# Optimization experiments

Measured on AMD Instinct MI355X. Metric: run time of the kernel, lower is better.

The kernel has to match this reference:

```python
import jax, jax.numpy as jnp
import numpy as np

ALPHA = 0.2  # LeakyReLU negative slope

def setup_inputs() -> dict:
    key = jax.random.key(0)
    k1, k2, k3 = jax.random.split(key, 3)
    B, N, D_in, D_out = 4, 512, 512, 256
    H = jax.random.normal(k1, (B, N, D_in), dtype=jnp.float32)
    # xavier-style scaled params
    W = jax.random.normal(k2, (D_out, D_in), dtype=jnp.float32) * (2.0 / (D_in + D_out)) ** 0.5
    a = jax.random.normal(k3, (D_out, 1), dtype=jnp.float32) * (2.0 / (D_out + 1)) ** 0.5
    return {"H": H, "W": W, "a": a}

def reference(H, W, a):
    # Wh: [B, N, D_out]
    Wh = jnp.einsum('bnd,od->bno', H, W)
    # additive pairwise scores: e[b,i,j] = leakyrelu(Wh[b,i]+Wh[b,j]) . a
    e = jnp.einsum('bijo,o->bij',
                   jax.nn.leaky_relu(Wh[:, :, None, :] + Wh[:, None, :, :], ALPHA),
                   a[:, 0])
    attention = jax.nn.softmax(e, axis=-1)          # [B, N, N]
    H_att = jnp.einsum('bij,bjo->bio', attention, Wh)  # [B, N, D_out]
    return H_att
```

## Files before the change

kernel.cpp:

```cpp
#include <hip/hip_runtime.h>

constexpr int Bq   = 4;
constexpr int Nq   = 512;
constexpr int DIN  = 512;
constexpr int DOUT = 256;

typedef _Float16 h2  __attribute__((ext_vector_type(2)));
typedef _Float16 h4  __attribute__((ext_vector_type(4)));
typedef _Float16 h8  __attribute__((ext_vector_type(8)));
typedef float    f4v __attribute__((ext_vector_type(4)));

#if defined(__has_builtin) && __has_builtin(__builtin_amdgcn_fdot2)
__device__ __forceinline__ float fdot2f(h2 a, h2 b, float c) {
    return __builtin_amdgcn_fdot2(a, b, c, false);
}
#else
__device__ __forceinline__ float fdot2f(h2 a, h2 b, float c) {
    return (float)a.x * (float)b.x + (float)a.y * (float)b.y + c;
}
#endif

__device__ __forceinline__ h8 cvt8(float4 lo, float4 hi) {
    h8 r;
    r[0] = (_Float16)lo.x; r[1] = (_Float16)lo.y;
    r[2] = (_Float16)lo.z; r[3] = (_Float16)lo.w;
    r[4] = (_Float16)hi.x; r[5] = (_Float16)hi.y;
    r[6] = (_Float16)hi.z; r[7] = (_Float16)hi.w;
    return r;
}

__global__ __launch_bounds__(256) void k1_wh(const float* __restrict__ H,
                                             const float* __restrict__ W,
                                             const float* __restrict__ a,
                                             h2* __restrict__ Wh16,
                                             h2* __restrict__ WhT16p,
                                             h2* __restrict__ WhT16n,
                                             h2* __restrict__ a16) {
    const int bid = blockIdx.x;
    const int t   = threadIdx.x;

    if (bid == 1024) {
        if (t < 64) {
            const int idx = 2 * t;
            const float4 v = *(const float4*)&a[2 * idx];
            h2 h0; h0.x = (_Float16)v.x; h0.y = (_Float16)v.y;
            h2 h1; h1.x = (_Float16)v.z; h1.y = (_Float16)v.w;
            a16[idx] = h0; a16[idx + 1] = h1;
        }
        return;
    }

    const int w    = t >> 6;
    const int lane = t & 63;
    const int T    = (bid << 1) | (w & 1);
    const int kh   = w >> 1;
    const int b    = (T >> 4) & 3;
    const int n0   = (T >> 6) << 4;
    const int o0   = (T & 15) << 4;
    const int quad = lane >> 4;
    const int col  = lane & 15;

    const float4* __restrict__ aP =
        (const float4*)(H + (size_t)(b * Nq + n0 + col) * DIN) + kh * 64 + quad * 2;
    const float4* __restrict__ bP =
        (const float4*)(W + (size_t)(o0 + col) * DIN) + kh * 64 + quad * 2;

    f4v acc = {0.f, 0.f, 0.f, 0.f};
    float4 fa0 = aP[0], fa1 = aP[1];
    float4 fb0 = bP[0], fb1 = bP[1];

#pragma unroll
    for (int kb = 0; kb < 8; ++kb) {
        float4 na0 = fa0, na1 = fa1, nb0 = fb0, nb1 = fb1;
        if (kb < 7) {
            na0 = aP[(kb + 1) * 8];
            na1 = aP[(kb + 1) * 8 + 1];
            nb0 = bP[(kb + 1) * 8];
            nb1 = bP[(kb + 1) * 8 + 1];
        }
        const h8 af = cvt8(fa0, fa1);
        const h8 bf = cvt8(fb0, fb1);
        acc = __builtin_amdgcn_mfma_f32_16x16x32_f16(af, bf, acc, 0, 0, 0);
        fa0 = na0; fa1 = na1; fb0 = nb0; fb1 = nb1;
    }

    __shared__ f4v sPart[2][64];
    if (kh) sPart[w & 1][lane] = acc;
    __syncthreads();
    if (!kh) {
        const f4v p = sPart[w & 1][lane];
#pragma unroll
        for (int r = 0; r < 4; ++r) acc[r] += p[r];

        const int rloc = n0 + quad * 4;

        h4 hj;
        hj[0] = (_Float16)acc[0]; hj[1] = (_Float16)acc[1];
        hj[2] = (_Float16)acc[2]; hj[3] = (_Float16)acc[3];
        *(h4*)(WhT16n + ((size_t)(b * 256 + o0 + col)) * 256 + (rloc >> 1)) = hj;

        h4* __restrict__ WhT16p4 = (h4*)WhT16p;
#pragma unroll
        for (int reg = 0; reg < 4; ++reg) {
            const float v  = acc[reg];
            const float vp = __shfl_xor(v, 1);
            h2 hv; hv.x = (_Float16)v; hv.y = (_Float16)vp;
            unsigned u;
            __builtin_memcpy(&u, &hv, 4);
            const unsigned u2 = __shfl_xor(u, 2);
            if ((col & 1) == 0) {
                const int o2 = (o0 + col) >> 1;
                Wh16[(size_t)(b * Nq + rloc + reg) * 128 + o2] = hv;
            }
            if ((col & 3) == 0) {
                h2 hv2;
                __builtin_memcpy(&hv2, &u2, 4);
                h4 q;
                q[0] = hv[0]; q[1] = hv[1]; q[2] = hv2[0]; q[3] = hv2[1];
                const int o4 = (o0 + col) >> 2;
                WhT16p4[(size_t)b * 32768 + (size_t)o4 * 512 + (rloc + reg)] = q;
            }
        }
    }
}

__global__ __launch_bounds__(1024, 8) void k23(const h2* __restrict__ Wh16,
                                               const h2* __restrict__ WhT16p,
                                               const h2* __restrict__ WhT16n,
                                               const h2* __restrict__ a16,
                                               float* __restrict__ out) {
    const int t   = threadIdx.x;
    const int blk = blockIdx.x;
    const int b   = blk & 3;
    const int i0  = (blk >> 2) << 2;

    __shared__ float smem[8192];
    __shared__ __align__(16) h2 sPh[4 * 272];
    __shared__ float wred[2][4][8];

    {
        const int h   = __builtin_amdgcn_readfirstlane(t >> 9);
        const int j   = t & 511;
        const int ob4 = h * 32;

        const h4* __restrict__ wjp  = (const h4*)WhT16p + (size_t)b * 32768 + j;
        const h4* __restrict__ wip4 = (const h4*)Wh16 + (size_t)(b * Nq + i0) * 64;
        const h4* __restrict__ a4p  = (const h4*)a16;

        float ab[4] = {0.f, 0.f, 0.f, 0.f};
        float rja = 0.f;
        h4 cA[8], cB[8];

#define K2_L8(buf, kb)                                                      \
    _Pragma("unroll") for (int s = 0; s < 8; ++s)                           \
        buf[s] = wjp[((size_t)(ob4 + (kb) + s)) * 512];

#define K2_C8(buf, kb)                                                      \
    _Pragma("unroll") for (int s = 0; s < 8; ++s) {                         \
        const int o4 = ob4 + (kb) + s;                                      \
        const h4 a4 = a4p[o4];                               \
        const h2 alo = __builtin_shufflevector(a4, a4, 0, 1);               \
        const h2 ahi = __builtin_shufflevector(a4, a4, 2, 3);               \
        const h4 c  = buf[s];                                               \
        const h2 clo = __builtin_shufflevector(c, c, 0, 1);                 \
        const h2 chi = __builtin_shufflevector(c, c, 2, 3);                 \
        rja = fdot2f(alo, clo, rja);                                        \
        rja = fdot2f(ahi, chi, rja);                                        \
        _Pragma("unroll") for (int rr = 0; rr < 4; ++rr) {                  \
            const h4 wi = wip4[rr * 64 + o4];                \
            const h2 wl = clo + __builtin_shufflevector(wi, wi, 0, 1);      \
            const h2 wh_ = chi + __builtin_shufflevector(wi, wi, 2, 3);     \
            const h2 awl = __builtin_elementwise_max(wl, -wl);              \
            const h2 awh = __builtin_elementwise_max(wh_, -wh_);            \
            ab[rr] = fdot2f(alo, awl, ab[rr]);                              \
            ab[rr] = fdot2f(ahi, awh, ab[rr]);                              \
        }                                                                   \
    }

        K2_L8(cA, 0)  K2_L8(cB, 8)
        K2_C8(cA, 0)  K2_L8(cA, 16)
        K2_C8(cB, 8)  K2_L8(cB, 24)
        K2_C8(cA, 16)
        K2_C8(cB, 24)
#undef K2_L8
#undef K2_C8

        float* sAb = smem;
        float* sRh = smem + 2048;
        float* sRf = smem + 2560;
        if (h == 1) {
#pragma unroll
            for (int rr = 0; rr < 4; ++rr) sAb[rr * 512 + j] = ab[rr];
            sRh[j] = rja;
        }
        __syncthreads();

        float rj = 0.f;
        if (h == 0) {
#pragma unroll
            for (int rr = 0; rr < 4; ++rr) ab[rr] += sAb[rr * 512 + j];
            rj = rja + sRh[j];
            sRf[j] = rj;
        }
        __syncthreads();

        float e[4], pv[4];
        const int lane = t & 63;
        const int w    = t >> 6;

        if (h == 0) {
#pragma unroll
            for (int rr = 0; rr < 4; ++rr)
                e[rr] = 0.6f * (sRf[i0 + rr] + rj) + 0.4f * ab[rr];
#pragma unroll
            for (int rr = 0; rr < 4; ++rr) {
                float v = e[rr];
#pragma unroll
                for (int off = 32; off > 0; off >>= 1) v = fmaxf(v, __shfl_xor(v, off));
                if (lane == 0) wred[0][rr][w] = v;
            }
        }
        __syncthreads();
        if (h == 0) {
#pragma unroll
            for (int rr = 0; rr < 4; ++rr) {
                const float4 q0 = *(const float4*)&wred[0][rr][0];
                const float4 q1 = *(const float4*)&wred[0][rr][4];
                const float m = fmaxf(fmaxf(fmaxf(q0.x, q0.y), fmaxf(q0.z, q0.w)),
                                      fmaxf(fmaxf(q1.x, q1.y), fmaxf(q1.z, q1.w)));
                pv[rr] = __expf(e[rr] - m);
            }
#pragma unroll
            for (int rr = 0; rr < 4; ++rr) {
                float v = pv[rr];
#pragma unroll
                for (int off = 32; off > 0; off >>= 1) v += __shfl_xor(v, off);
                if (lane == 0) wred[1][rr][w] = v;
            }
        }
        __syncthreads();
        if (h == 0) {
#pragma unroll
            for (int rr = 0; rr < 4; ++rr) {
                const float4 q0 = *(const float4*)&wred[1][rr][0];
                const float4 q1 = *(const float4*)&wred[1][rr][4];
                const float s = (q0.x + q0.y + q0.z + q0.w) + (q1.x + q1.y + q1.z + q1.w);
                const float pn = pv[rr] * (1.0f / s);
                const float pp = __shfl_xor(pn, 1);
                if ((j & 1) == 0) {
                    h2 hv; hv.x = (_Float16)pn; hv.y = (_Float16)pp;
                    sPh[rr * 272 + (j >> 1)] = hv;
                }
            }
        }
        __syncthreads();
    }

    {
        const int w16  = __builtin_amdgcn_readfirstlane(t >> 6);
        const int lane = t & 63;
        const int quad = lane >> 4;
        const int col  = lane & 15;
        const int o0   = w16 << 4;

        const h2* __restrict__ wt =
            WhT16n + (size_t)b * 65536 + (size_t)(o0 + col) * 256 + quad * 4;
        const h2* __restrict__ ap = sPh + (col & 3) * 272 + quad * 4;

        f4v acc = {0.f, 0.f, 0.f, 0.f};
        h8 b0 = *(const h8*)wt;
#pragma unroll
        for (int kb = 0; kb < 16; ++kb) {
            h8 b1 = b0;
            if (kb < 15) b1 = *(const h8*)(wt + (kb + 1) * 16);
            const h8 af = *(const h8*)(ap + kb * 16);
            acc = __builtin_amdgcn_mfma_f32_16x16x32_f16(af, b0, acc, 0, 0, 0);
            b0 = b1;
        }

        if (quad == 0) {
#pragma unroll
            for (int reg = 0; reg < 4; ++reg) {
                out[((size_t)(b * Nq) + i0 + reg) * DOUT + o0 + col] = acc[reg];
            }
        }
    }
}

extern "C" void kernel_launch(void* const* d_in, const int* in_sizes, int n_in,
                              void* d_out, int out_size, void* d_ws, size_t ws_size,
                              hipStream_t stream) {
    const float* H = (const float*)d_in[0];
    const float* W = (const float*)d_in[1];
    const float* a = (const float*)d_in[2];
    float* out = (float*)d_out;

    h2* Wh16   = (h2*)d_ws;
    h2* WhT16p = Wh16 + 262144;
    h2* WhT16n = WhT16p + 262144;
    h2* a16    = WhT16n + 262144;

    hipLaunchKernelGGL(k1_wh, dim3(1025), dim3(256),  0, stream, H, W, a, Wh16, WhT16p, WhT16n, a16);
    hipLaunchKernelGGL(k23,   dim3(512),  dim3(1024), 0, stream, Wh16, WhT16p, WhT16n, a16, out);
}
```

Measured before the change: 106.7 us.

## Exploit symmetry of pairwise scores and split score and softmax kernels

The pairwise |Wh_i+Wh_j|·a term is symmetric, so each block now computes it only for the next 256 columns after its 4 rows and writes both E[i,j] and E[j,i]. The 4x4 diagonal block and the per-row r terms are handled by spare warps. A new kernel reads E and r, does the softmax and runs the P·Wh product. This roughly halves the dominant pairwise compute, at the cost of an extra launch and a global E buffer round trip of about 4 MB.

Result: no change. 105.8 us (-0.8%).

```diff
diff --git a/kernel.cpp b/kernel.cpp
--- a/kernel.cpp
+++ b/kernel.cpp
@@ -124,48 +124,44 @@
     }
 }
 
-__global__ __launch_bounds__(1024, 8) void k23(const h2* __restrict__ Wh16,
-                                               const h2* __restrict__ WhT16p,
-                                               const h2* __restrict__ WhT16n,
-                                               const h2* __restrict__ a16,
-                                               float* __restrict__ out) {
+__global__ __launch_bounds__(1024, 8) void kA(const h2* __restrict__ Wh16,
+                                              const h2* __restrict__ WhT16p,
+                                              const h2* __restrict__ a16,
+                                              float* __restrict__ E,
+                                              float* __restrict__ r) {
     const int t   = threadIdx.x;
     const int blk = blockIdx.x;
     const int b   = blk & 3;
-    const int i0  = (blk >> 2) << 2;
-
-    __shared__ float smem[8192];
-    __shared__ __align__(16) h2 sPh[4 * 272];
-    __shared__ float wred[2][4][8];
-
-    {
-        const int h   = __builtin_amdgcn_readfirstlane(t >> 9);
-        const int j   = t & 511;
-        const int ob4 = h * 32;
-
-        const h4* __restrict__ wjp  = (const h4*)WhT16p + (size_t)b * 32768 + j;
-        const h4* __restrict__ wip4 = (const h4*)Wh16 + (size_t)(b * Nq + i0) * 64;
-        const h4* __restrict__ a4p  = (const h4*)a16;
-
-        float ab[4] = {0.f, 0.f, 0.f, 0.f};
-        float rja = 0.f;
-        h4 cA[8], cB[8];
-
-#define K2_L8(buf, kb)                                                      \
+    const int u   = blk >> 2;
+    const int i0  = u << 2;
+
+    __shared__ float sAb[4 * 4 * 256];
+
+    const int oq  = __builtin_amdgcn_readfirstlane(t >> 8);
+    const int j8  = t & 255;
+    const int j   = (i0 + 4 + j8) & 511;
+    const int ob0 = oq << 4;
+
+    const h4* __restrict__ wjpB = (const h4*)WhT16p + (size_t)b * 32768 + j;
+    const h4* __restrict__ wip4 = (const h4*)Wh16 + (size_t)(b * Nq + i0) * 64;
+    const h4* __restrict__ a4p  = (const h4*)a16;
+
+    float ab[4] = {0.f, 0.f, 0.f, 0.f};
+    h4 cA[8], cB[8];
+
+#define KA_L8(buf, kb)                                                      \
     _Pragma("unroll") for (int s = 0; s < 8; ++s)                           \
-        buf[s] = wjp[((size_t)(ob4 + (kb) + s)) * 512];
-
-#define K2_C8(buf, kb)                                                      \
+        buf[s] = wjpB[(size_t)(ob0 + (kb) + s) * 512];
+
+#define KA_C8(buf, kb)                                                      \
     _Pragma("unroll") for (int s = 0; s < 8; ++s) {                         \
-        const int o4 = ob4 + (kb) + s;                                      \
+        const int o4 = ob0 + (kb) + s;                                      \
         const h4 a4 = a4p[o4];                               \
         const h2 alo = __builtin_shufflevector(a4, a4, 0, 1);               \
         const h2 ahi = __builtin_shufflevector(a4, a4, 2, 3);               \
         const h4 c  = buf[s];                                               \
         const h2 clo = __builtin_shufflevector(c, c, 0, 1);                 \
         const h2 chi = __builtin_shufflevector(c, c, 2, 3);                 \
-        rja = fdot2f(alo, clo, rja);                                        \
-        rja = fdot2f(ahi, chi, rja);                                        \
         _Pragma("unroll") for (int rr = 0; rr < 4; ++rr) {                  \
             const h4 wi = wip4[rr * 64 + o4];                \
             const h2 wl = clo + __builtin_shufflevector(wi, wi, 0, 1);      \
@@ -177,80 +173,131 @@
         }                                                                   \
     }
 
-        K2_L8(cA, 0)  K2_L8(cB, 8)
-        K2_C8(cA, 0)  K2_L8(cA, 16)
-        K2_C8(cB, 8)  K2_L8(cB, 24)
-        K2_C8(cA, 16)
-        K2_C8(cB, 24)
-#undef K2_L8
-#undef K2_C8
-
-        float* sAb = smem;
-        float* sRh = smem + 2048;
-        float* sRf = smem + 2560;
-        if (h == 1) {
-#pragma unroll
-            for (int rr = 0; rr < 4; ++rr) sAb[rr * 512 + j] = ab[rr];
-            sRh[j] = rja;
-        }
-        __syncthreads();
-
-        float rj = 0.f;
-        if (h == 0) {
-#pragma unroll
-            for (int rr = 0; rr < 4; ++rr) ab[rr] += sAb[rr * 512 + j];
-            rj = rja + sRh[j];
-            sRf[j] = rj;
-        }
-        __syncthreads();
-
-        float e[4], pv[4];
+    KA_L8(cA, 0) KA_L8(cB, 8)
+    KA_C8(cA, 0)
+    KA_C8(cB, 8)
+#undef KA_L8
+#undef KA_C8
+
+#pragma unroll
+    for (int rr = 0; rr < 4; ++rr) sAb[(rr * 4 + oq) * 256 + j8] = ab[rr];
+    __syncthreads();
+
+    if (t < 256) {
+        float v[4];
+#pragma unroll
+        for (int rr = 0; rr < 4; ++rr)
+            v[rr] = 0.4f * (sAb[(rr * 4 + 0) * 256 + t] + sAb[(rr * 4 + 1) * 256 + t] +
+                            sAb[(rr * 4 + 2) * 256 + t] + sAb[(rr * 4 + 3) * 256 + t]);
+        const int jj = (i0 + 4 + t) & 511;
+#pragma unroll
+        for (int rr = 0; rr < 4; ++rr)
+            E[((size_t)(b * Nq) + i0 + rr) * 512 + jj] = v[rr];
+        float4 f;
+        f.x = v[0]; f.y = v[1]; f.z = v[2]; f.w = v[3];
+        *(float4*)&E[((size_t)(b * Nq) + jj) * 512 + i0] = f;
+    } else if (t < 320) {
+        const int l = t & 63;
+        const h4 a4 = a4p[l];
+        const h2 alo = __builtin_shufflevector(a4, a4, 0, 1);
+        const h2 ahi = __builtin_shufflevector(a4, a4, 2, 3);
+        h4 wrow[4];
+#pragma unroll
+        for (int rr = 0; rr < 4; ++rr) wrow[rr] = wip4[rr * 64 + l];
+#pragma unroll
+        for (int p = 0; p < 4; ++p)
+#pragma unroll
+            for (int q = p; q < 4; ++q) {
+                const h4 ws = wrow[p] + wrow[q];
+                const h4 aw = __builtin_elementwise_max(ws, -ws);
+                float s = fdot2f(alo, __builtin_shufflevector(aw, aw, 0, 1),
+                          fdot2f(ahi, __builtin_shufflevector(aw, aw, 2, 3), 0.f));
+#pragma unroll
+                for (int off = 32; off > 0; off >>= 1) s += __shfl_xor(s, off);
+                if (l == 0) {
+                    const float val = 0.4f * s;
+                    E[((size_t)(b * Nq) + i0 + p) * 512 + i0 + q] = val;
+                    E[((size_t)(b * Nq) + i0 + q) * 512 + i0 + p] = val;
+                }
+            }
+    } else if (t < 384) {
+        const int l = t & 63;
+        const h4 a4 = a4p[l];
+        const h2 alo = __builtin_shufflevector(a4, a4, 0, 1);
+        const h2 ahi = __builtin_shufflevector(a4, a4, 2, 3);
+#pragma unroll
+        for (int rr = 0; rr < 4; ++rr) {
+            const h4 wi = wip4[rr * 64 + l];
+            float s = fdot2f(alo, __builtin_shufflevector(wi, wi, 0, 1),
+                      fdot2f(ahi, __builtin_shufflevector(wi, wi, 2, 3), 0.f));
+#pragma unroll
+            for (int off = 32; off > 0; off >>= 1) s += __shfl_xor(s, off);
+            if (l == 0) r[b * Nq + i0 + rr] = s;
+        }
+    }
+}
+
+__global__ __launch_bounds__(1024, 8) void kB(const float* __restrict__ E,
+                                              const float* __restrict__ r,
+                                              const h2* __restrict__ WhT16n,
+                                              float* __restrict__ out) {
+    const int t   = threadIdx.x;
+    const int blk = blockIdx.x;
+    const int b   = blk & 3;
+    const int i0  = (blk >> 2) << 2;
+
+    __shared__ __align__(16) h2 sPh[4 * 272];
+    __shared__ float wred[2][4][8];
+
+    {
+        const int j    = t & 511;
+        const int rh   = __builtin_amdgcn_readfirstlane(t >> 9);
         const int lane = t & 63;
         const int w    = t >> 6;
-
-        if (h == 0) {
-#pragma unroll
-            for (int rr = 0; rr < 4; ++rr)
-                e[rr] = 0.6f * (sRf[i0 + rr] + rj) + 0.4f * ab[rr];
-#pragma unroll
-            for (int rr = 0; rr < 4; ++rr) {
-                float v = e[rr];
-#pragma unroll
-                for (int off = 32; off > 0; off >>= 1) v = fmaxf(v, __shfl_xor(v, off));
-                if (lane == 0) wred[0][rr][w] = v;
-            }
+        const int slot = w & 7;
+
+        const float rj = r[b * Nq + j];
+        float e[2], pv[2];
+#pragma unroll
+        for (int rr = 0; rr < 2; ++rr) {
+            const int row = rh * 2 + rr;
+            const float ri = r[b * Nq + i0 + row];
+            e[rr] = 0.6f * (ri + rj) + E[((size_t)(b * Nq) + i0 + row) * 512 + j];
+        }
+
+#pragma unroll
+        for (int rr = 0; rr < 2; ++rr) {
+            float v = e[rr];
+#pragma unroll
+            for (int off = 32; off > 0; off >>= 1) v = fmaxf(v, __shfl_xor(v, off));
+            if (lane == 0) wred[0][rh * 2 + rr][slot] = v;
         }
         __syncthreads();
-        if (h == 0) {
-#pragma unroll
-            for (int rr = 0; rr < 4; ++rr) {
-                const float4 q0 = *(const float4*)&wred[0][rr][0];
-                const float4 q1 = *(const float4*)&wred[0][rr][4];
-                const float m = fmaxf(fmaxf(fmaxf(q0.x, q0.y), fmaxf(q0.z, q0.w)),
-                                      fmaxf(fmaxf(q1.x, q1.y), fmaxf(q1.z, q1.w)));
-                pv[rr] = __expf(e[rr] - m);
-            }
-#pragma unroll
-            for (int rr = 0; rr < 4; ++rr) {
-                float v = pv[rr];
-#pragma unroll
-                for (int off = 32; off > 0; off >>= 1) v += __shfl_xor(v, off);
-                if (lane == 0) wred[1][rr][w] = v;
-            }
+#pragma unroll
+        for (int rr = 0; rr < 2; ++rr) {
+            const int row = rh * 2 + rr;
+            const float4 q0 = *(const float4*)&wred[0][row][0];
+            const float4 q1 = *(const float4*)&wred[0][row][4];
+            const float m = fmaxf(fmaxf(fmaxf(q0.x, q0.y), fmaxf(q0.z, q0.w)),
+                                  fmaxf(fmaxf(q1.x, q1.y), fmaxf(q1.z, q1.w)));
+            pv[rr] = __expf(e[rr] - m);
+            float v = pv[rr];
+#pragma unroll
+            for (int off = 32; off > 0; off >>= 1) v += __shfl_xor(v, off);
+            if (lane == 0) wred[1][row][slot] = v;
         }
         __syncthreads();
-        if (h == 0) {
-#pragma unroll
-            for (int rr = 0; rr < 4; ++rr) {
-                const float4 q0 = *(const float4*)&wred[1][rr][0];
-                const float4 q1 = *(const float4*)&wred[1][rr][4];
-                const float s = (q0.x + q0.y + q0.z + q0.w) + (q1.x + q1.y + q1.z + q1.w);
-                const float pn = pv[rr] * (1.0f / s);
-                const float pp = __shfl_xor(pn, 1);
-                if ((j & 1) == 0) {
-                    h2 hv; hv.x = (_Float16)pn; hv.y = (_Float16)pp;
-                    sPh[rr * 272 + (j >> 1)] = hv;
-                }
+#pragma unroll
+        for (int rr = 0; rr < 2; ++rr) {
+            const int row = rh * 2 + rr;
+            const float4 q0 = *(const float4*)&wred[1][row][0];
+            const float4 q1 = *(const float4*)&wred[1][row][4];
+            const float s = (q0.x + q0.y + q0.z + q0.w) + (q1.x + q1.y + q1.z + q1.w);
+            const float pn = pv[rr] * (1.0f / s);
+            const float pp = __shfl_xor(pn, 1);
+            if ((j & 1) == 0) {
+                h2 hv; hv.x = (_Float16)pn; hv.y = (_Float16)pp;
+                sPh[row * 272 + (j >> 1)] = hv;
             }
         }
         __syncthreads();
@@ -299,7 +346,12 @@
     h2* WhT16p = Wh16 + 262144;
     h2* WhT16n = WhT16p + 262144;
     h2* a16    = WhT16n + 262144;
+    float* E   = (float*)(a16 + 128);
+    float* r   = E + (size_t)Bq * Nq * Nq / Nq * Nq;
+
+    r = E + 1048576;
 
     hipLaunchKernelGGL(k1_wh, dim3(1025), dim3(256),  0, stream, H, W, a, Wh16, WhT16p, WhT16n, a16);
-    hipLaunchKernelGGL(k23,   dim3(512),  dim3(1024), 0, stream, Wh16, WhT16p, WhT16n, a16, out);
-}
+    hipLaunchKernelGGL(kA,    dim3(512),  dim3(1024), 0, stream, Wh16, WhT16p, a16, E, r);
+    hipLaunchKernelGGL(kB,    dim3(512),  dim3(1024), 0, stream, E, r, WhT16n, out);
+}
```
